# Kernel optimization log

Hardware: AMD Instinct MI355X
Metric: run time of the kernel (lower is better)

## Reference

```python
import jax, jax.numpy as jnp
import numpy as np
from jax import lax

SPATIAL = 4
PAD = 1
STRIDE = 1


def _route(x, rconv_w, rconv_b, fc_w, fc_b, num_experts):
    # x: (b, c, h, w); adaptive avg pool to (SPATIAL, SPATIAL) -- h,w divisible by SPATIAL
    b, c, h, w = x.shape
    pooled = x.reshape(b, c, SPATIAL, h // SPATIAL, SPATIAL, w // SPATIAL).mean(axis=(3, 5))
    # 1x1 conv: (b,c,s,s) x (rc,c) -> (b,rc,s,s)
    y = jnp.einsum('bcij,rc->brij', pooled, rconv_w) + rconv_b[None, :, None, None]
    y = jax.nn.relu(y).reshape(b, -1)                      # (b, rc*s*s)
    y = jax.nn.relu(y @ fc_w.T + fc_b)                     # (b, num_experts*c)
    y = y.reshape(b, num_experts, c)
    return jax.nn.sigmoid(y)                               # (b, k, c)


def _conv_per_sample(xi, wi):
    # xi: (c_in, h, w), wi: (c_out, c_in, kh, kw)
    out = lax.conv_general_dilated(
        xi[None], wi, window_strides=(STRIDE, STRIDE),
        padding=[(PAD, PAD), (PAD, PAD)],
        dimension_numbers=('NCHW', 'OIHW', 'NCHW'))
    return out[0]


def setup_inputs() -> dict:
    key = jax.random.key(0)
    ks = jax.random.split(key, 6)
    b, c_in, c_out, kk, ne = 16, 256, 256, 3, 3
    rc = max(c_in // 16, 16)  # reduction_channels = 16
    x = jax.random.normal(ks[0], (b, c_in, 64, 64), dtype=jnp.float32)
    expert_weight = jax.random.normal(ks[1], (ne, c_out, c_in, kk, kk), dtype=jnp.float32) * 0.02
    rconv_w = jax.random.normal(ks[2], (rc, c_in), dtype=jnp.float32) * 0.05
    rconv_b = jax.random.normal(ks[3], (rc,), dtype=jnp.float32) * 0.05
    fc_w = jax.random.normal(ks[4], (ne * c_in, rc * SPATIAL * SPATIAL), dtype=jnp.float32) * 0.05
    fc_b = jax.random.normal(ks[5], (ne * c_in,), dtype=jnp.float32) * 0.05
    return {"x": x, "expert_weight": expert_weight, "rconv_w": rconv_w,
            "rconv_b": rconv_b, "fc_w": fc_w, "fc_b": fc_b}


def reference(x, expert_weight, rconv_w, rconv_b, fc_w, fc_b):
    ne = expert_weight.shape[0]
    r = _route(x, rconv_w, rconv_b, fc_w, fc_b, ne)        # (b, k, c_in)
    # per-sample combined weights: routing scales input channels of each expert kernel
    w = jnp.einsum('bkc,kocij->bocij', r, expert_weight)    # (b, c_out, c_in, kh, kw)
    out = jax.vmap(_conv_per_sample)(x, w)                  # (b, c_out, h', w')
    return out
```

## Files before the change

kernel.cpp:

```cpp
#include <hip/hip_runtime.h>

#define B_   16
#define C_   256
#define OC_  256
#define H_   64
#define W_   64

typedef __attribute__((ext_vector_type(8))) __bf16 bf16x8;
typedef __attribute__((ext_vector_type(4))) float  f32x4;

__device__ __forceinline__ short f2bf(float f) {
    unsigned u = __float_as_uint(f);
    u += 0x7fffu + ((u >> 16) & 1u);
    return (short)(u >> 16);
}
__device__ __forceinline__ unsigned pk2(float a, float b) {
    return (unsigned(f2bf(a)) & 0xffffu) | (unsigned(f2bf(b)) << 16);
}
__device__ __forceinline__ void gll16(const void* g, void* l) {
    __builtin_amdgcn_global_load_lds(
        (const __attribute__((address_space(1))) unsigned int*)g,
        (__attribute__((address_space(3))) unsigned int*)l,
        16, 0, 0);
}

__global__ __launch_bounds__(256) void k_transpose_pool(
        const float* __restrict__ x, short* __restrict__ xt, float* __restrict__ pooled) {
    int y = blockIdx.x, b = blockIdx.y, t = threadIdx.x;
    int si = y >> 4;
    int lane = t & 63, wv = t >> 6;
    int xq = lane & 15, cw = lane >> 4;
    __shared__ float tile[64 * 67];

    for (int cc = 0; cc < 4; ++cc) {
        int cbase = cc * 64;
        if (cc) __syncthreads();
        #pragma unroll
        for (int r = 0; r < 4; ++r) {
            int c_l = r * 16 + wv * 4 + cw;
            float4 v = *(const float4*)&x[(((size_t)b * C_ + cbase + c_l) * H_ + y) * W_ + xq * 4];
            float* tp = &tile[c_l * 67 + xq * 4];
            tp[0] = v.x; tp[1] = v.y; tp[2] = v.z; tp[3] = v.w;
            float s = v.x + v.y + v.z + v.w;
            s += __shfl_xor(s, 1);
            s += __shfl_xor(s, 2);
            if ((lane & 3) == 0)
                atomicAdd(&pooled[((b * 4 + si) * 4 + (xq >> 2)) * 256 + cbase + c_l], s);
        }
        __syncthreads();
        #pragma unroll
        for (int r2 = 0; r2 < 2; ++r2) {
            int u = r2 * 256 + t;
            int xx = u >> 3, cgl = u & 7;
            float f[8];
            #pragma unroll
            for (int j = 0; j < 8; ++j) f[j] = tile[(cgl * 8 + j) * 67 + xx];
            uint4 pkv;
            pkv.x = pk2(f[0], f[1]); pkv.y = pk2(f[2], f[3]);
            pkv.z = pk2(f[4], f[5]); pkv.w = pk2(f[6], f[7]);
            *(uint4*)&xt[(((size_t)b * H_ + y) * W_ + xx) * C_ + cbase + cgl * 8] = pkv;
        }
    }
}

__global__ __launch_bounds__(256) void k_route(
        const float* __restrict__ pooled, const float* __restrict__ rconv_w,
        const float* __restrict__ rconv_b, const float* __restrict__ fc_w,
        const float* __restrict__ fc_b, float* __restrict__ r_buf) {
    int b = blockIdx.x;
    int t = threadIdx.x;
    __shared__ float pl[16][257];
    __shared__ float y1[256];

    #pragma unroll
    for (int q = 0; q < 16; ++q)
        pl[q][t] = pooled[b * 4096 + q * 256 + t] * (1.0f / 256.0f);
    __syncthreads();
    {
        int rcc = t >> 4, ss = t & 15;
        float acc = rconv_b[rcc];
        #pragma unroll 8
        for (int c = 0; c < 256; ++c)
            acc += pl[ss][c] * rconv_w[rcc * 256 + c];
        y1[rcc * 16 + ss] = fmaxf(acc, 0.f);
    }
    __syncthreads();
    for (int e0 = 0; e0 < 768; e0 += 256) {
        int e = e0 + t;
        float acc = fc_b[e];
        #pragma unroll 8
        for (int q = 0; q < 256; ++q)
            acc += y1[q] * fc_w[(size_t)e * 256 + q];
        acc = fmaxf(acc, 0.f);
        r_buf[(size_t)b * 768 + e] = 1.f / (1.f + __expf(-acc));
    }
}

__global__ __launch_bounds__(256) void k_combine(
        const float* __restrict__ E, const float* __restrict__ r_buf,
        short* __restrict__ wcomb) {
    int o = blockIdx.x;
    int b0 = blockIdx.y * 4;
    int t = threadIdx.x;
    __shared__ float eT[3][2304];
    #pragma unroll
    for (int k = 0; k < 3; ++k)
        #pragma unroll
        for (int q = 0; q < 9; ++q)
            eT[k][q * 256 + t] = E[((size_t)k * OC_ + o) * 2304 + q * 256 + t];
    __syncthreads();
    int c = t;
    #pragma unroll
    for (int bb = 0; bb < 4; ++bb) {
        int b = b0 + bb;
        float r0 = r_buf[(size_t)b * 768 + c];
        float r1 = r_buf[(size_t)b * 768 + 256 + c];
        float r2 = r_buf[(size_t)b * 768 + 512 + c];
        short* wo = wcomb + ((size_t)(b * OC_ + o) * 9) * C_;
        #pragma unroll
        for (int tap = 0; tap < 9; ++tap) {
            float v = r0 * eT[0][c * 9 + tap] + r1 * eT[1][c * 9 + tap]
                    + r2 * eT[2][c * 9 + tap];
            wo[tap * C_ + c] = f2bf(v);
        }
    }
}

__global__ __launch_bounds__(256, 2) void k_conv(
        const short* __restrict__ xt, const short* __restrict__ wcomb,
        float* __restrict__ out, const short* __restrict__ zbuf) {
    int lin  = blockIdx.x;
    int work = (lin & 7) * 128 + (lin >> 3);
    int b      = work >> 6;
    int o_base = ((work >> 5) & 1) * 128;
    int y0     = (work & 31) * 2;

    int t = threadIdx.x;
    int lane = t & 63, w = t >> 6;
    int quad = lane >> 4, l15 = lane & 15;

    __shared__ __align__(16) short win[4 * 64 * 64];
    __shared__ __align__(16) short abuf[2][128 * 64];

    const short* wsrc[8];
    #pragma unroll
    for (int r = 0; r < 8; ++r) {
        int u = r * 256 + t;
        int pos = u >> 3, sp = u & 7;
        int wrow = pos >> 6, xc = pos & 63;
        int yy = y0 - 1 + wrow;
        int ss = sp ^ (xc & 7);
        wsrc[r] = ((unsigned)yy < 64u)
            ? xt + (((size_t)b * 64 + yy) * 64 + xc) * 256 + ss * 8
            : zbuf;
    }
    const short* asrc[4];
    #pragma unroll
    for (int r = 0; r < 4; ++r) {
        int u = r * 256 + t;
        int o_l = u >> 3, sp = u & 7;
        int ss = sp ^ (o_l & 7);
        asrc[r] = wcomb + (((size_t)b * 256 + o_base + o_l) * 9) * 256 + ss * 8;
    }

    int m_base = (w & 1) * 64;
    int n_base = (w >> 1) * 64;
    int ry0 = n_base >> 6;
    int xb[4];
    #pragma unroll
    for (int nb = 0; nb < 4; ++nb) xb[nb] = nb * 16 + l15;

    f32x4 acc[4][4];
    #pragma unroll
    for (int i = 0; i < 4; ++i)
        #pragma unroll
        for (int j = 0; j < 4; ++j) acc[i][j] = {0.f, 0.f, 0.f, 0.f};

    for (int cc = 0; cc < 4; ++cc) {
        int ccOff = cc * 64;
        #pragma unroll
        for (int r = 0; r < 8; ++r)
            gll16(wsrc[r] + ccOff, &win[(r * 256 + w * 64) * 8]);
        #pragma unroll
        for (int r = 0; r < 4; ++r)
            gll16(asrc[r] + ccOff, &abuf[0][(r * 256 + w * 64) * 8]);
        __syncthreads();

        #pragma unroll
        for (int tap = 0; tap < 9; ++tap) {
            const int ti = tap / 3, tj = tap % 3;
            const int cur = tap & 1;
            if (tap < 8) {
                int off2 = (tap + 1) * 256 + ccOff;
                #pragma unroll
                for (int r = 0; r < 4; ++r)
                    gll16(asrc[r] + off2, &abuf[cur ^ 1][(r * 256 + w * 64) * 8]);
            }
            int wrb = (ry0 + ti) * 4096;
            #pragma unroll
            for (int s = 0; s < 2; ++s) {
                int slog = s * 4 + quad;
                bf16x8 af[4], bv[4];
                #pragma unroll
                for (int mb = 0; mb < 4; ++mb) {
                    int o_l = m_base + mb * 16 + l15;
                    af[mb] = *(const bf16x8*)&abuf[cur][o_l * 64 + ((slog ^ (o_l & 7)) * 8)];
                }
                #pragma unroll
                for (int nb = 0; nb < 4; ++nb) {
                    int xc = xb[nb] + (tj - 1);
                    bool ok = ((unsigned)xc < 64u);
                    int xs = ok ? xc : 0;
                    bf16x8 v = *(const bf16x8*)&win[wrb + xs * 64 + ((slog ^ (xs & 7)) * 8)];
                    bf16x8 zz = {};
                    bv[nb] = ok ? v : zz;
                }
                #pragma unroll
                for (int mb = 0; mb < 4; ++mb)
                    #pragma unroll
                    for (int nb = 0; nb < 4; ++nb)
                        acc[mb][nb] = __builtin_amdgcn_mfma_f32_16x16x32_bf16(
                            af[mb], bv[nb], acc[mb][nb], 0, 0, 0);
            }
            __syncthreads();
        }
    }

    #pragma unroll
    for (int mb = 0; mb < 4; ++mb) {
        #pragma unroll
        for (int nb = 0; nb < 4; ++nb) {
            int p  = n_base + nb * 16 + l15;
            int yy = y0 + (p >> 6);
            int xx = p & 63;
            #pragma unroll
            for (int rg = 0; rg < 4; ++rg) {
                int o = o_base + m_base + mb * 16 + quad * 4 + rg;
                out[(((size_t)b * OC_ + o) * H_ + yy) * W_ + xx] = acc[mb][nb][rg];
            }
        }
    }
}

extern "C" void kernel_launch(void* const* d_in, const int* in_sizes, int n_in,
                              void* d_out, int out_size, void* d_ws, size_t ws_size,
                              hipStream_t stream) {
    const float* x       = (const float*)d_in[0];
    const float* E       = (const float*)d_in[1];
    const float* rconv_w = (const float*)d_in[2];
    const float* rconv_b = (const float*)d_in[3];
    const float* fc_w    = (const float*)d_in[4];
    const float* fc_b    = (const float*)d_in[5];
    float* out = (float*)d_out;

    char* ws = (char*)d_ws;
    short* xt     = (short*)(ws);
    short* wcomb  = (short*)(ws + 33554432);
    float* pooled = (float*)(ws + 52428800);
    short* zbuf   = (short*)(ws + 52690944);
    float* rbuf   = (float*)(ws + 52692992);

    hipMemsetAsync(pooled, 0, 262144 + 1024, stream);

    k_transpose_pool<<<dim3(64, 16), 256, 0, stream>>>(x, xt, pooled);
    k_route<<<dim3(16), 256, 0, stream>>>(pooled, rconv_w, rconv_b, fc_w, fc_b, rbuf);
    k_combine<<<dim3(256, 4), 256, 0, stream>>>(E, rbuf, wcomb);
    k_conv<<<dim3(1024), 256, 0, stream>>>(xt, wcomb, out, zbuf);
}
```

Measured before the change: 242.7 us.

## Load conv weight fragments directly to registers and drop per-tap barriers

The conv kernel no longer stages the combined weights through a double-buffered LDS tile. Each lane now loads its A fragments straight from global memory into registers, prefetching two phases ahead. This removes the per-tap __syncthreads and frees LDS so the launch bound can rise to 3 blocks per CU, and MFMA sections get a raised s_setprio. The cost is redundant global loads of weights across waves, higher register pressure, and exposed global latency if the prefetch distance is too short.

```diff
diff --git a/kernel.cpp b/kernel.cpp
--- a/kernel.cpp
+++ b/kernel.cpp
@@ -126,7 +126,7 @@
     }
 }
 
-__global__ __launch_bounds__(256, 2) void k_conv(
+__global__ __launch_bounds__(256, 3) void k_conv(
         const short* __restrict__ xt, const short* __restrict__ wcomb,
         float* __restrict__ out, const short* __restrict__ zbuf) {
     int lin  = blockIdx.x;
@@ -140,7 +140,6 @@
     int quad = lane >> 4, l15 = lane & 15;
 
     __shared__ __align__(16) short win[4 * 64 * 64];
-    __shared__ __align__(16) short abuf[2][128 * 64];
 
     const short* wsrc[8];
     #pragma unroll
@@ -154,21 +153,17 @@
             ? xt + (((size_t)b * 64 + yy) * 64 + xc) * 256 + ss * 8
             : zbuf;
     }
-    const short* asrc[4];
-    #pragma unroll
-    for (int r = 0; r < 4; ++r) {
-        int u = r * 256 + t;
-        int o_l = u >> 3, sp = u & 7;
-        int ss = sp ^ (o_l & 7);
-        asrc[r] = wcomb + (((size_t)b * 256 + o_base + o_l) * 9) * 256 + ss * 8;
-    }
 
     int m_base = (w & 1) * 64;
     int n_base = (w >> 1) * 64;
     int ry0 = n_base >> 6;
-    int xb[4];
-    #pragma unroll
-    for (int nb = 0; nb < 4; ++nb) xb[nb] = nb * 16 + l15;
+
+    const short* pA[4];
+    #pragma unroll
+    for (int mb = 0; mb < 4; ++mb) {
+        int o_l = m_base + mb * 16 + l15;
+        pA[mb] = wcomb + ((size_t)(b * 256 + o_base + o_l) * 9) * 256 + quad * 8;
+    }
 
     f32x4 acc[4][4];
     #pragma unroll
@@ -181,49 +176,50 @@
         #pragma unroll
         for (int r = 0; r < 8; ++r)
             gll16(wsrc[r] + ccOff, &win[(r * 256 + w * 64) * 8]);
-        #pragma unroll
-        for (int r = 0; r < 4; ++r)
-            gll16(asrc[r] + ccOff, &abuf[0][(r * 256 + w * 64) * 8]);
+
+        bf16x8 P[2][4];
+        #pragma unroll
+        for (int mb = 0; mb < 4; ++mb) {
+            P[0][mb] = *(const bf16x8*)(pA[mb] + ccOff);
+            P[1][mb] = *(const bf16x8*)(pA[mb] + ccOff + 32);
+        }
         __syncthreads();
 
         #pragma unroll
-        for (int tap = 0; tap < 9; ++tap) {
-            const int ti = tap / 3, tj = tap % 3;
-            const int cur = tap & 1;
-            if (tap < 8) {
-                int off2 = (tap + 1) * 256 + ccOff;
+        for (int ph = 0; ph < 18; ++ph) {
+            const int tp = ph >> 1, s = ph & 1;
+            const int ti = tp / 3, tj = tp % 3;
+            const int cur = ph & 1;
+            int wrb = (ry0 + ti) * 4096;
+
+            bf16x8 bv[4];
+            #pragma unroll
+            for (int nb = 0; nb < 4; ++nb) {
+                int xc = nb * 16 + l15 + (tj - 1);
+                bool ok = ((unsigned)xc < 64u);
+                int xs = ok ? xc : 0;
+                int slog = s * 4 + quad;
+                bf16x8 v = *(const bf16x8*)&win[wrb + xs * 64 + ((slog ^ (xs & 7)) * 8)];
+                bf16x8 zz = {};
+                bv[nb] = ok ? v : zz;
+            }
+            __builtin_amdgcn_s_setprio(1);
+            #pragma unroll
+            for (int mb = 0; mb < 4; ++mb)
                 #pragma unroll
-                for (int r = 0; r < 4; ++r)
-                    gll16(asrc[r] + off2, &abuf[cur ^ 1][(r * 256 + w * 64) * 8]);
-            }
-            int wrb = (ry0 + ti) * 4096;
-            #pragma unroll
-            for (int s = 0; s < 2; ++s) {
-                int slog = s * 4 + quad;
-                bf16x8 af[4], bv[4];
-                #pragma unroll
-                for (int mb = 0; mb < 4; ++mb) {
-                    int o_l = m_base + mb * 16 + l15;
-                    af[mb] = *(const bf16x8*)&abuf[cur][o_l * 64 + ((slog ^ (o_l & 7)) * 8)];
-                }
-                #pragma unroll
-                for (int nb = 0; nb < 4; ++nb) {
-                    int xc = xb[nb] + (tj - 1);
-                    bool ok = ((unsigned)xc < 64u);
-                    int xs = ok ? xc : 0;
-                    bf16x8 v = *(const bf16x8*)&win[wrb + xs * 64 + ((slog ^ (xs & 7)) * 8)];
-                    bf16x8 zz = {};
-                    bv[nb] = ok ? v : zz;
-                }
+                for (int nb = 0; nb < 4; ++nb)
+                    acc[mb][nb] = __builtin_amdgcn_mfma_f32_16x16x32_bf16(
+                        P[cur][mb], bv[nb], acc[mb][nb], 0, 0, 0);
+            __builtin_amdgcn_s_setprio(0);
+
+            if (ph < 16) {
+                const int np = ph + 2, ntp = np >> 1, ns = np & 1;
                 #pragma unroll
                 for (int mb = 0; mb < 4; ++mb)
-                    #pragma unroll
-                    for (int nb = 0; nb < 4; ++nb)
-                        acc[mb][nb] = __builtin_amdgcn_mfma_f32_16x16x32_bf16(
-                            af[mb], bv[nb], acc[mb][nb], 0, 0, 0);
+                    P[cur][mb] = *(const bf16x8*)(pA[mb] + ntp * 256 + ccOff + ns * 32);
             }
-            __syncthreads();
-        }
+        }
+        if (cc < 3) __syncthreads();
     }
 
     #pragma unroll
```

After: 313.6 us. +29.2%, slower.

## Enlarge conv tile to four rows and parallelize routing FC across wavefronts

Applied to the files above, without the earlier changes.

The conv kernel now computes four output rows per block instead of two. The block loads a 6-row input window and each wave keeps an 4x8 MFMA accumulator tile, so every weight tile read from LDS is reused across twice as many pixels and the grid is halved. Pointer arrays are replaced with 32-bit offsets to save registers, and the MFMA burst is wrapped in s_setprio. The routing FC is split into four slices per sample, with one wavefront reduction per output row, so fc_w reads are coalesced. The cost is higher register and LDS pressure in the conv kernel, which may lower occupancy, and fewer blocks for 256 CUs.

```diff
diff --git a/kernel.cpp b/kernel.cpp
--- a/kernel.cpp
+++ b/kernel.cpp
@@ -67,8 +67,10 @@
         const float* __restrict__ pooled, const float* __restrict__ rconv_w,
         const float* __restrict__ rconv_b, const float* __restrict__ fc_w,
         const float* __restrict__ fc_b, float* __restrict__ r_buf) {
-    int b = blockIdx.x;
+    int b = blockIdx.x >> 2;
+    int slice = blockIdx.x & 3;
     int t = threadIdx.x;
+    int lane = t & 63, wv = t >> 6;
     __shared__ float pl[16][257];
     __shared__ float y1[256];
 
@@ -85,14 +87,21 @@
         y1[rcc * 16 + ss] = fmaxf(acc, 0.f);
     }
     __syncthreads();
-    for (int e0 = 0; e0 < 768; e0 += 256) {
-        int e = e0 + t;
-        float acc = fc_b[e];
-        #pragma unroll 8
-        for (int q = 0; q < 256; ++q)
-            acc += y1[q] * fc_w[(size_t)e * 256 + q];
-        acc = fmaxf(acc, 0.f);
-        r_buf[(size_t)b * 768 + e] = 1.f / (1.f + __expf(-acc));
+    #pragma unroll 4
+    for (int i = 0; i < 48; ++i) {
+        int e = slice * 192 + wv * 48 + i;
+        const float* row = fc_w + (size_t)e * 256;
+        float p = y1[lane]       * row[lane]
+                + y1[lane + 64]  * row[lane + 64]
+                + y1[lane + 128] * row[lane + 128]
+                + y1[lane + 192] * row[lane + 192];
+        #pragma unroll
+        for (int d = 1; d < 64; d <<= 1)
+            p += __shfl_xor(p, d);
+        if (lane == 0) {
+            float a = fmaxf(p + fc_b[e], 0.f);
+            r_buf[(size_t)b * 768 + e] = 1.f / (1.f + __expf(-a));
+        }
     }
 }
 
@@ -130,60 +139,58 @@
         const short* __restrict__ xt, const short* __restrict__ wcomb,
         float* __restrict__ out, const short* __restrict__ zbuf) {
     int lin  = blockIdx.x;
-    int work = (lin & 7) * 128 + (lin >> 3);
-    int b      = work >> 6;
-    int o_base = ((work >> 5) & 1) * 128;
-    int y0     = (work & 31) * 2;
+    int work = (lin & 7) * 64 + (lin >> 3);
+    int b      = work >> 5;
+    int o_base = ((work >> 4) & 1) * 128;
+    int y0     = (work & 15) * 4;
 
     int t = threadIdx.x;
     int lane = t & 63, w = t >> 6;
     int quad = lane >> 4, l15 = lane & 15;
 
-    __shared__ __align__(16) short win[4 * 64 * 64];
+    __shared__ __align__(16) short win[6 * 64 * 64];
     __shared__ __align__(16) short abuf[2][128 * 64];
 
-    const short* wsrc[8];
-    #pragma unroll
-    for (int r = 0; r < 8; ++r) {
+    int zoff = (int)(zbuf - xt);
+
+    int woff[12];
+    #pragma unroll
+    for (int r = 0; r < 12; ++r) {
         int u = r * 256 + t;
         int pos = u >> 3, sp = u & 7;
         int wrow = pos >> 6, xc = pos & 63;
         int yy = y0 - 1 + wrow;
         int ss = sp ^ (xc & 7);
-        wsrc[r] = ((unsigned)yy < 64u)
-            ? xt + (((size_t)b * 64 + yy) * 64 + xc) * 256 + ss * 8
-            : zbuf;
-    }
-    const short* asrc[4];
+        woff[r] = ((unsigned)yy < 64u)
+            ? ((b * 64 + yy) * 64 + xc) * 256 + ss * 8
+            : zoff;
+    }
+    int aoff[4];
     #pragma unroll
     for (int r = 0; r < 4; ++r) {
         int u = r * 256 + t;
         int o_l = u >> 3, sp = u & 7;
         int ss = sp ^ (o_l & 7);
-        asrc[r] = wcomb + (((size_t)b * 256 + o_base + o_l) * 9) * 256 + ss * 8;
+        aoff[r] = ((b * 256 + o_base + o_l) * 9) * 256 + ss * 8;
     }
 
     int m_base = (w & 1) * 64;
-    int n_base = (w >> 1) * 64;
-    int ry0 = n_base >> 6;
-    int xb[4];
-    #pragma unroll
-    for (int nb = 0; nb < 4; ++nb) xb[nb] = nb * 16 + l15;
-
-    f32x4 acc[4][4];
+    int ry0    = (w >> 1) * 2;
+
+    f32x4 acc[4][8];
     #pragma unroll
     for (int i = 0; i < 4; ++i)
         #pragma unroll
-        for (int j = 0; j < 4; ++j) acc[i][j] = {0.f, 0.f, 0.f, 0.f};
+        for (int j = 0; j < 8; ++j) acc[i][j] = {0.f, 0.f, 0.f, 0.f};
 
     for (int cc = 0; cc < 4; ++cc) {
         int ccOff = cc * 64;
         #pragma unroll
-        for (int r = 0; r < 8; ++r)
-            gll16(wsrc[r] + ccOff, &win[(r * 256 + w * 64) * 8]);
+        for (int r = 0; r < 12; ++r)
+            gll16(xt + woff[r] + ccOff, &win[(r * 256 + w * 64) * 8]);
         #pragma unroll
         for (int r = 0; r < 4; ++r)
-            gll16(asrc[r] + ccOff, &abuf[0][(r * 256 + w * 64) * 8]);
+            gll16(wcomb + aoff[r] + ccOff, &abuf[0][(r * 256 + w * 64) * 8]);
         __syncthreads();
 
         #pragma unroll
@@ -194,33 +201,37 @@
                 int off2 = (tap + 1) * 256 + ccOff;
                 #pragma unroll
                 for (int r = 0; r < 4; ++r)
-                    gll16(asrc[r] + off2, &abuf[cur ^ 1][(r * 256 + w * 64) * 8]);
+                    gll16(wcomb + aoff[r] + off2, &abuf[cur ^ 1][(r * 256 + w * 64) * 8]);
             }
-            int wrb = (ry0 + ti) * 4096;
             #pragma unroll
             for (int s = 0; s < 2; ++s) {
                 int slog = s * 4 + quad;
-                bf16x8 af[4], bv[4];
+                bf16x8 af[4], bv[8];
                 #pragma unroll
                 for (int mb = 0; mb < 4; ++mb) {
                     int o_l = m_base + mb * 16 + l15;
                     af[mb] = *(const bf16x8*)&abuf[cur][o_l * 64 + ((slog ^ (o_l & 7)) * 8)];
                 }
                 #pragma unroll
-                for (int nb = 0; nb < 4; ++nb) {
-                    int xc = xb[nb] + (tj - 1);
+                for (int nb = 0; nb < 8; ++nb) {
+                    int rr = nb >> 2, xq4 = nb & 3;
+                    int xc = xq4 * 16 + l15 + (tj - 1);
                     bool ok = ((unsigned)xc < 64u);
                     int xs = ok ? xc : 0;
-                    bf16x8 v = *(const bf16x8*)&win[wrb + xs * 64 + ((slog ^ (xs & 7)) * 8)];
+                    int wrow = ry0 + rr + ti;
+                    bf16x8 v = *(const bf16x8*)&win[(wrow * 64 + xs) * 64
+                                                    + ((slog ^ (xs & 7)) * 8)];
                     bf16x8 zz = {};
                     bv[nb] = ok ? v : zz;
                 }
+                __builtin_amdgcn_s_setprio(1);
                 #pragma unroll
                 for (int mb = 0; mb < 4; ++mb)
                     #pragma unroll
-                    for (int nb = 0; nb < 4; ++nb)
+                    for (int nb = 0; nb < 8; ++nb)
                         acc[mb][nb] = __builtin_amdgcn_mfma_f32_16x16x32_bf16(
                             af[mb], bv[nb], acc[mb][nb], 0, 0, 0);
+                __builtin_amdgcn_s_setprio(0);
             }
             __syncthreads();
         }
@@ -229,10 +240,10 @@
     #pragma unroll
     for (int mb = 0; mb < 4; ++mb) {
         #pragma unroll
-        for (int nb = 0; nb < 4; ++nb) {
-            int p  = n_base + nb * 16 + l15;
-            int yy = y0 + (p >> 6);
-            int xx = p & 63;
+        for (int nb = 0; nb < 8; ++nb) {
+            int rr = nb >> 2, xq4 = nb & 3;
+            int xx = xq4 * 16 + l15;
+            int yy = y0 + ry0 + rr;
             #pragma unroll
             for (int rg = 0; rg < 4; ++rg) {
                 int o = o_base + m_base + mb * 16 + quad * 4 + rg;
@@ -263,7 +274,7 @@
     hipMemsetAsync(pooled, 0, 262144 + 1024, stream);
 
     k_transpose_pool<<<dim3(64, 16), 256, 0, stream>>>(x, xt, pooled);
-    k_route<<<dim3(16), 256, 0, stream>>>(pooled, rconv_w, rconv_b, fc_w, fc_b, rbuf);
+    k_route<<<dim3(64), 256, 0, stream>>>(pooled, rconv_w, rconv_b, fc_w, fc_b, rbuf);
     k_combine<<<dim3(256, 4), 256, 0, stream>>>(E, rbuf, wcomb);
-    k_conv<<<dim3(1024), 256, 0, stream>>>(xt, wcomb, out, zbuf);
-}
+    k_conv<<<dim3(512), 256, 0, stream>>>(xt, wcomb, out, zbuf);
+}
```

After: 251.4 us. 3.6% more time.
